# Performance work log

Measured on AMD Instinct MI355X. Metric: run time of the kernel, lower is better.

The kernel has to match this reference:

```python
import jax, jax.numpy as jnp
import numpy as np

T, LDIMS, HID, HID2 = 768, 256, 512, 512


def setup_inputs() -> dict:
    key = jax.random.key(0)
    ks = jax.random.split(key, 8)
    s = 0.05  # small init scale keeps tanh out of saturation
    return {
        "x": jax.random.normal(ks[0], (T, 2, LDIMS), dtype=jnp.float32),
        "hidLayerFOH": jax.random.normal(ks[1], (2 * LDIMS, HID), dtype=jnp.float32) * s,
        "hidLayerFOM": jax.random.normal(ks[2], (2 * LDIMS, HID), dtype=jnp.float32) * s,
        "catBias": jax.random.normal(ks[3], (2 * HID,), dtype=jnp.float32) * s,
        "hid2Layer": jax.random.normal(ks[4], (2 * HID, HID2), dtype=jnp.float32) * s,
        "hid2Bias": jax.random.normal(ks[5], (HID2,), dtype=jnp.float32) * s,
        "outLayer": jax.random.normal(ks[6], (HID2, 1), dtype=jnp.float32) * s,
        "outBias": jax.random.normal(ks[7], (1,), dtype=jnp.float32) * s,
    }


def reference(x, hidLayerFOH, hidLayerFOM, catBias, hid2Layer, hid2Bias, outLayer, outBias):
    # x: [T, 2, ldims] -> concat forward/backward LSTM states -> [T, 2*ldims]
    xc = x.reshape(x.shape[0], -1)
    Hf = xc @ hidLayerFOH  # [T, HID] headfov per token
    Mf = xc @ hidLayerFOM  # [T, HID] modfov per token
    # Original: tanh(concat([headfov_i, modfov_j]) + catBias) @ hid2Layer.
    # tanh is elementwise, so split the concat: act halves separately, then
    # split hid2Layer into top/bottom blocks — same math, no [T,T,2H] tensor.
    actH = jnp.tanh(Hf + catBias[:HID])   # [T, HID]
    actM = jnp.tanh(Mf + catBias[HID:])   # [T, HID]
    AH = actH @ hid2Layer[:HID]           # [T, HID2]
    AM = actM @ hid2Layer[HID:]           # [T, HID2]
    # Pairwise second layer: Z[i,j] = tanh(AH[i] + AM[j] + hid2Bias)
    Z = jnp.tanh(AH[:, None, :] + AM[None, :, :] + hid2Bias)  # [T, T, HID2]
    scores = jnp.einsum("ijh,h->ij", Z, outLayer[:, 0]) + outBias[0]  # [T, T]
    return scores
```

## Files before the change

### kernel.cpp

```cpp
#include <hip/hip_runtime.h>

#define TT 768
#define KD 512
#define NC 1024
#define RLN2_2 2.8853900817779268f

typedef short short8 __attribute__((ext_vector_type(8)));
typedef float f32x4  __attribute__((ext_vector_type(4)));
typedef float f32x2  __attribute__((ext_vector_type(2)));

__device__ __forceinline__ float fast_exp2(float x) {
#if __has_builtin(__builtin_amdgcn_exp2f)
    return __builtin_amdgcn_exp2f(x);
#else
    return exp2f(x);
#endif
}
__device__ __forceinline__ float fast_rcp(float x) {
#if __has_builtin(__builtin_amdgcn_rcpf)
    return __builtin_amdgcn_rcpf(x);
#else
    return 1.0f / x;
#endif
}
__device__ __forceinline__ float fast_tanh(float x) {
    float e = fast_exp2(x * RLN2_2);
    return fmaf(-2.0f, fast_rcp(e + 1.0f), 1.0f);
}
__device__ __forceinline__ ushort f2bf(float f) {
    uint u = __float_as_uint(f);
    u += 0x7fff + ((u >> 16) & 1);
    return (ushort)(u >> 16);
}

__global__ __launch_bounds__(64) void k_prep(
    const float* __restrict__ x, const float* __restrict__ foh,
    const float* __restrict__ fom, const float* __restrict__ hid2,
    ushort* __restrict__ xb, ushort* __restrict__ b1t, ushort* __restrict__ h2t)
{
    const int b = blockIdx.x, lane = threadIdx.x;
    if (b < 384) {
        int base = b * 1024 + lane * 16;
        #pragma unroll
        for (int q = 0; q < 4; ++q) {
            float4 v = *(const float4*)&x[base + q * 4];
            ushort4 o; o.x = f2bf(v.x); o.y = f2bf(v.y); o.z = f2bf(v.z); o.w = f2bf(v.w);
            *(ushort4*)&xb[base + q * 4] = o;
        }
        return;
    }
    __shared__ float tile[32][33];
    int bb = b - 384;
    const float* src; ushort* dst; int R, C;
    if (bb < 256)      { src = foh;  dst = b1t;             R = 512;  C = 512; }
    else if (bb < 512) { src = fom;  dst = b1t + 512 * 512; R = 512;  C = 512; bb -= 256; }
    else               { src = hid2; dst = h2t;             R = 1024; C = 512; bb -= 512; }
    const int r0 = (bb >> 4) * 32, c0 = (bb & 15) * 32;
    const int ty = lane >> 3, tx = lane & 7;
    #pragma unroll
    for (int q = 0; q < 4; ++q) {
        float4 v = *(const float4*)&src[(r0 + ty + q * 8) * C + c0 + tx * 4];
        tile[ty + q * 8][tx * 4 + 0] = v.x;
        tile[ty + q * 8][tx * 4 + 1] = v.y;
        tile[ty + q * 8][tx * 4 + 2] = v.z;
        tile[ty + q * 8][tx * 4 + 3] = v.w;
    }
    __syncthreads();
    #pragma unroll
    for (int q = 0; q < 4; ++q) {
        int cl = ty + q * 8;
        ushort4 o;
        o.x = f2bf(tile[tx * 4 + 0][cl]);
        o.y = f2bf(tile[tx * 4 + 1][cl]);
        o.z = f2bf(tile[tx * 4 + 2][cl]);
        o.w = f2bf(tile[tx * 4 + 3][cl]);
        *(ushort4*)&dst[(c0 + cl) * R + r0 + tx * 4] = o;
    }
}

__global__ __launch_bounds__(128) void k_gemm1(
    const ushort* __restrict__ xb, const ushort* __restrict__ b1t,
    const float* __restrict__ catBias, ushort* __restrict__ act)
{
    __shared__ float ps[64][20];
    const int t = threadIdx.x;
    const int kv = t >> 6, lane = t & 63;
    const int n0 = blockIdx.x * 32;
    const int m0 = blockIdx.y * 32;
    const int lrow = lane & 15, lk = (lane >> 4) * 8;
    const int kbase = kv * 256;

    const ushort* pa0 = &xb[(m0 + lrow) * KD + kbase + lk];
    const ushort* pa1 = pa0 + 16 * KD;
    const ushort* pb0 = &b1t[(n0 + lrow) * KD + kbase + lk];
    const ushort* pb1 = pb0 + 16 * KD;

    f32x4 acc[2][2] = {};
    #pragma unroll 4
    for (int k0 = 0; k0 < 256; k0 += 32) {
        short8 a0 = *(const short8*)(pa0 + k0);
        short8 a1 = *(const short8*)(pa1 + k0);
        short8 b0 = *(const short8*)(pb0 + k0);
        short8 b1 = *(const short8*)(pb1 + k0);
        acc[0][0] = __builtin_amdgcn_mfma_f32_16x16x32_bf16(a0, b0, acc[0][0], 0, 0, 0);
        acc[0][1] = __builtin_amdgcn_mfma_f32_16x16x32_bf16(a0, b1, acc[0][1], 0, 0, 0);
        acc[1][0] = __builtin_amdgcn_mfma_f32_16x16x32_bf16(a1, b0, acc[1][0], 0, 0, 0);
        acc[1][1] = __builtin_amdgcn_mfma_f32_16x16x32_bf16(a1, b1, acc[1][1], 0, 0, 0);
    }
    if (kv == 1) {
        *(f32x4*)&ps[lane][0]  = acc[0][0];
        *(f32x4*)&ps[lane][4]  = acc[0][1];
        *(f32x4*)&ps[lane][8]  = acc[1][0];
        *(f32x4*)&ps[lane][12] = acc[1][1];
    }
    __syncthreads();
    if (kv == 0) {
        acc[0][0] += *(const f32x4*)&ps[lane][0];
        acc[0][1] += *(const f32x4*)&ps[lane][4];
        acc[1][0] += *(const f32x4*)&ps[lane][8];
        acc[1][1] += *(const f32x4*)&ps[lane][12];
        const int crow = (lane >> 4) * 4, ccol = lane & 15;
        #pragma unroll
        for (int nf = 0; nf < 2; ++nf) {
            int col = n0 + nf * 16 + ccol;
            float cb = catBias[col];
            #pragma unroll
            for (int mf = 0; mf < 2; ++mf) {
                #pragma unroll
                for (int r = 0; r < 4; ++r) {
                    int row = m0 + mf * 16 + crow + r;
                    act[row * NC + col] = f2bf(fast_tanh(acc[mf][nf][r] + cb));
                }
            }
        }
    }
}

__global__ __launch_bounds__(128) void k_gemm2(
    const ushort* __restrict__ act, const ushort* __restrict__ h2t,
    const float* __restrict__ hid2Bias, float* __restrict__ pw)
{
    __shared__ float ps[64][20];
    const int t = threadIdx.x;
    const int kv = t >> 6, lane = t & 63;
    const int n0 = blockIdx.x * 32;
    const int m0 = blockIdx.y * 32;
    const bool top = (blockIdx.x < 16);
    const int koff = top ? 0 : 512;
    const int nc0  = top ? n0 : n0 - 512;
    const int lrow = lane & 15, lk = (lane >> 4) * 8;
    const int kbase = kv * 256;

    const ushort* pa0 = &act[(m0 + lrow) * NC + koff + kbase + lk];
    const ushort* pa1 = pa0 + 16 * NC;
    const ushort* pb0 = &h2t[(nc0 + lrow) * NC + koff + kbase + lk];
    const ushort* pb1 = pb0 + 16 * NC;

    f32x4 acc[2][2] = {};
    #pragma unroll 4
    for (int k0 = 0; k0 < 256; k0 += 32) {
        short8 a0 = *(const short8*)(pa0 + k0);
        short8 a1 = *(const short8*)(pa1 + k0);
        short8 b0 = *(const short8*)(pb0 + k0);
        short8 b1 = *(const short8*)(pb1 + k0);
        acc[0][0] = __builtin_amdgcn_mfma_f32_16x16x32_bf16(a0, b0, acc[0][0], 0, 0, 0);
        acc[0][1] = __builtin_amdgcn_mfma_f32_16x16x32_bf16(a0, b1, acc[0][1], 0, 0, 0);
        acc[1][0] = __builtin_amdgcn_mfma_f32_16x16x32_bf16(a1, b0, acc[1][0], 0, 0, 0);
        acc[1][1] = __builtin_amdgcn_mfma_f32_16x16x32_bf16(a1, b1, acc[1][1], 0, 0, 0);
    }
    if (kv == 1) {
        *(f32x4*)&ps[lane][0]  = acc[0][0];
        *(f32x4*)&ps[lane][4]  = acc[0][1];
        *(f32x4*)&ps[lane][8]  = acc[1][0];
        *(f32x4*)&ps[lane][12] = acc[1][1];
    }
    __syncthreads();
    if (kv == 0) {
        acc[0][0] += *(const f32x4*)&ps[lane][0];
        acc[0][1] += *(const f32x4*)&ps[lane][4];
        acc[1][0] += *(const f32x4*)&ps[lane][8];
        acc[1][1] += *(const f32x4*)&ps[lane][12];
        const int crow = (lane >> 4) * 4, ccol = lane & 15;
        #pragma unroll
        for (int nf = 0; nf < 2; ++nf) {
            int col = n0 + nf * 16 + ccol;
            float hb = top ? hid2Bias[col] : 0.0f;
            #pragma unroll
            for (int mf = 0; mf < 2; ++mf) {
                #pragma unroll
                for (int r = 0; r < 4; ++r) {
                    int row = m0 + mf * 16 + crow + r;
                    pw[row * NC + col] = fast_exp2(RLN2_2 * (acc[mf][nf][r] + hb));
                }
            }
        }
    }
}

__global__ __launch_bounds__(256) void k_pair(
    const float* __restrict__ pw, const float* __restrict__ w,
    const float* __restrict__ outBias, float* __restrict__ out)
{
    __shared__ float Ea[4][16][18];
    __shared__ float Em[4][16][18];
    __shared__ float wl[512];

    const int t    = threadIdx.x;
    const int wv   = t >> 6, lane = t & 63;
    const int bid  = blockIdx.x;
    const int sw   = (bid & 7) * 288 + (bid >> 3);
    const int it = sw / 48, jt = sw % 48;
    const int i0 = it * 16, j0 = jt * 16;
    const int hb0 = wv * 128;

    *(float2*)&wl[hb0 + lane * 2] = *(const float2*)&w[hb0 + lane * 2];
    float4 wa = *(const float4*)&w[lane * 8];
    float4 wb = *(const float4*)&w[lane * 8 + 4];
    float lsum = (wa.x + wa.y) + (wa.z + wa.w) + (wb.x + wb.y) + (wb.z + wb.w);
    #pragma unroll
    for (int d = 1; d < 64; d <<= 1) lsum += __shfl_xor(lsum, d, 64);

    const int sr = lane >> 2;
    const int sc = (lane & 3) * 4;
    const float* srcA = &pw[(i0 + sr) * NC + hb0 + sc];
    const float* srcM = &pw[(j0 + sr) * NC + 512 + hb0 + sc];

    const int li = lane >> 3, lj = lane & 7;

    float4 fa = *(const float4*)(srcA);
    float4 fm = *(const float4*)(srcM);

    const f32x2 one2 = {1.0f, 1.0f};
    f32x2 accA[2] = {}, accB[2] = {};

    #pragma unroll 1
    for (int c = 0; c < 8; ++c) {
        const int hh = c * 16;
        *(float4*)&Ea[wv][sr][sc] = fa;
        *(float4*)&Em[wv][sr][sc] = fm;
        if (c < 7) {
            fa = *(const float4*)(srcA + hh + 16);
            fm = *(const float4*)(srcM + hh + 16);
        }
        #pragma unroll
        for (int hq = 0; hq < 4; ++hq) {
            float4 e0 = *(const float4*)&Ea[wv][2 * li    ][hq * 4];
            float4 e1 = *(const float4*)&Ea[wv][2 * li + 1][hq * 4];
            float4 f0 = *(const float4*)&Em[wv][2 * lj    ][hq * 4];
            float4 f1 = *(const float4*)&Em[wv][2 * lj + 1][hq * 4];
            float4 w4 = *(const float4*)&wl[hb0 + hh + hq * 4];
            #define PKQUAD(DA, DB, WH, ACCA, ACCB)                   \
            {                                                        \
                f32x2 Q  = DA * DB;                                  \
                float pr = Q.x * Q.y;                                \
                float R  = fast_rcp(pr);                             \
                float RW = R * (WH);                                 \
                f32x2 T  = (f32x2){Q.y, Q.x} * RW;                   \
                ACCA = __builtin_elementwise_fma(T, DB, ACCA);       \
                ACCB = __builtin_elementwise_fma(T, DA, ACCB);       \
            }
            #define HSTEP(H, S)                                                     \
            {                                                                       \
                f32x2 F  = {f0.H, f1.H};                                            \
                f32x2 D0 = __builtin_elementwise_fma((f32x2){e0.H, e0.H}, F, one2); \
                f32x2 D1 = __builtin_elementwise_fma((f32x2){e1.H, e1.H}, F, one2); \
                PKQUAD(D0, D1, w4.H, accA[S], accB[S])                              \
            }
            HSTEP(x, 0) HSTEP(y, 1) HSTEP(z, 0) HSTEP(w, 1)
            #undef HSTEP
            #undef PKQUAD
        }
    }

    f32x2 s0 = accA[0] + accA[1];
    f32x2 s1 = accB[0] + accB[1];

    float* partial = (float*)Ea;
    __syncthreads();
    if (wv >= 1) {
        float* p = partial + (wv - 1) * 256 + lane * 4;
        p[0] = s0.x; p[1] = s0.y; p[2] = s1.x; p[3] = s1.y;
    }
    __syncthreads();
    if (wv == 0) {
        const float base = lsum + outBias[0];
        float t00 = s0.x, t01 = s0.y, t10 = s1.x, t11 = s1.y;
        #pragma unroll
        for (int q = 0; q < 3; ++q) {
            const float* p = partial + q * 256 + lane * 4;
            t00 += p[0]; t01 += p[1]; t10 += p[2]; t11 += p[3];
        }
        const int gi = i0 + 2 * li, gj = j0 + 2 * lj;
        float2 o0, o1;
        o0.x = fmaf(-2.f, t00, base);
        o0.y = fmaf(-2.f, t01, base);
        o1.x = fmaf(-2.f, t10, base);
        o1.y = fmaf(-2.f, t11, base);
        *(float2*)&out[gi * TT + gj]       = o0;
        *(float2*)&out[(gi + 1) * TT + gj] = o1;
    }
}

extern "C" void kernel_launch(void* const* d_in, const int* in_sizes, int n_in,
                              void* d_out, int out_size, void* d_ws, size_t ws_size,
                              hipStream_t stream) {
    const float* x        = (const float*)d_in[0];
    const float* foh      = (const float*)d_in[1];
    const float* fom      = (const float*)d_in[2];
    const float* catBias  = (const float*)d_in[3];
    const float* hid2     = (const float*)d_in[4];
    const float* hid2Bias = (const float*)d_in[5];
    const float* outLayer = (const float*)d_in[6];
    const float* outBias  = (const float*)d_in[7];
    float* out = (float*)d_out;

    char* wsb = (char*)d_ws;
    float*  pw  = (float*)(wsb);
    ushort* act = (ushort*)(wsb + 3145728);
    ushort* xb  = (ushort*)(wsb + 4718592);
    ushort* b1t = (ushort*)(wsb + 5505024);
    ushort* h2t = (ushort*)(wsb + 6553600);

    k_prep <<<dim3(1408),    64, 0, stream>>>(x, foh, fom, hid2, xb, b1t, h2t);
    k_gemm1<<<dim3(32, 24), 128, 0, stream>>>(xb, b1t, catBias, act);
    k_gemm2<<<dim3(32, 24), 128, 0, stream>>>(act, h2t, hid2Bias, pw);
    k_pair <<<dim3(2304),   256, 0, stream>>>(pw, outLayer, outBias, out);
}
```

Measured before the change: 58.84 us.

## Fuse bf16 conversion and weight transpose into GEMM loads, drop prep kernel

Removes the separate prep kernel that converted x and the weight matrices to bf16 and transposed them. Each GEMM now reads the fp32 weights directly, stages a 32x32 tile per wave in shared memory, and converts to bf16 while gathering the transposed MFMA operands; gemm1 also converts x on the fly. This cuts one kernel launch and the round trip of the converted copies through global memory. In exchange, the conversion and transpose are repeated in every row-block, and the k-loop is no longer unrolled, so load latency is less hidden.

```diff
diff --git a/kernel.cpp b/kernel.cpp
--- a/kernel.cpp
+++ b/kernel.cpp
@@ -33,79 +33,65 @@
     return (ushort)(u >> 16);
 }
 
-__global__ __launch_bounds__(64) void k_prep(
+__global__ __launch_bounds__(128) void k_gemm1(
     const float* __restrict__ x, const float* __restrict__ foh,
-    const float* __restrict__ fom, const float* __restrict__ hid2,
-    ushort* __restrict__ xb, ushort* __restrict__ b1t, ushort* __restrict__ h2t)
-{
-    const int b = blockIdx.x, lane = threadIdx.x;
-    if (b < 384) {
-        int base = b * 1024 + lane * 16;
-        #pragma unroll
-        for (int q = 0; q < 4; ++q) {
-            float4 v = *(const float4*)&x[base + q * 4];
-            ushort4 o; o.x = f2bf(v.x); o.y = f2bf(v.y); o.z = f2bf(v.z); o.w = f2bf(v.w);
-            *(ushort4*)&xb[base + q * 4] = o;
-        }
-        return;
-    }
-    __shared__ float tile[32][33];
-    int bb = b - 384;
-    const float* src; ushort* dst; int R, C;
-    if (bb < 256)      { src = foh;  dst = b1t;             R = 512;  C = 512; }
-    else if (bb < 512) { src = fom;  dst = b1t + 512 * 512; R = 512;  C = 512; bb -= 256; }
-    else               { src = hid2; dst = h2t;             R = 1024; C = 512; bb -= 512; }
-    const int r0 = (bb >> 4) * 32, c0 = (bb & 15) * 32;
-    const int ty = lane >> 3, tx = lane & 7;
-    #pragma unroll
-    for (int q = 0; q < 4; ++q) {
-        float4 v = *(const float4*)&src[(r0 + ty + q * 8) * C + c0 + tx * 4];
-        tile[ty + q * 8][tx * 4 + 0] = v.x;
-        tile[ty + q * 8][tx * 4 + 1] = v.y;
-        tile[ty + q * 8][tx * 4 + 2] = v.z;
-        tile[ty + q * 8][tx * 4 + 3] = v.w;
-    }
-    __syncthreads();
-    #pragma unroll
-    for (int q = 0; q < 4; ++q) {
-        int cl = ty + q * 8;
-        ushort4 o;
-        o.x = f2bf(tile[tx * 4 + 0][cl]);
-        o.y = f2bf(tile[tx * 4 + 1][cl]);
-        o.z = f2bf(tile[tx * 4 + 2][cl]);
-        o.w = f2bf(tile[tx * 4 + 3][cl]);
-        *(ushort4*)&dst[(c0 + cl) * R + r0 + tx * 4] = o;
-    }
-}
-
-__global__ __launch_bounds__(128) void k_gemm1(
-    const ushort* __restrict__ xb, const ushort* __restrict__ b1t,
-    const float* __restrict__ catBias, ushort* __restrict__ act)
+    const float* __restrict__ fom, const float* __restrict__ catBias,
+    ushort* __restrict__ act)
 {
     __shared__ float ps[64][20];
+    __shared__ float bt[2][32][33];
+
     const int t = threadIdx.x;
     const int kv = t >> 6, lane = t & 63;
     const int n0 = blockIdx.x * 32;
     const int m0 = blockIdx.y * 32;
+    const float* B = (n0 < 512) ? foh : fom;
+    const int nc0  = (n0 < 512) ? n0 : n0 - 512;
     const int lrow = lane & 15, lk = (lane >> 4) * 8;
     const int kbase = kv * 256;
 
-    const ushort* pa0 = &xb[(m0 + lrow) * KD + kbase + lk];
-    const ushort* pa1 = pa0 + 16 * KD;
-    const ushort* pb0 = &b1t[(n0 + lrow) * KD + kbase + lk];
-    const ushort* pb1 = pb0 + 16 * KD;
+    const int skr = lane >> 1;
+    const int snc = (lane & 1) * 16;
+
+    const float* px0 = &x[(m0 + lrow) * KD + kbase + lk];
+    const float* px1 = px0 + 16 * KD;
 
     f32x4 acc[2][2] = {};
-    #pragma unroll 4
-    for (int k0 = 0; k0 < 256; k0 += 32) {
-        short8 a0 = *(const short8*)(pa0 + k0);
-        short8 a1 = *(const short8*)(pa1 + k0);
-        short8 b0 = *(const short8*)(pb0 + k0);
-        short8 b1 = *(const short8*)(pb1 + k0);
-        acc[0][0] = __builtin_amdgcn_mfma_f32_16x16x32_bf16(a0, b0, acc[0][0], 0, 0, 0);
-        acc[0][1] = __builtin_amdgcn_mfma_f32_16x16x32_bf16(a0, b1, acc[0][1], 0, 0, 0);
-        acc[1][0] = __builtin_amdgcn_mfma_f32_16x16x32_bf16(a1, b0, acc[1][0], 0, 0, 0);
-        acc[1][1] = __builtin_amdgcn_mfma_f32_16x16x32_bf16(a1, b1, acc[1][1], 0, 0, 0);
+    #pragma unroll 1
+    for (int c = 0; c < 8; ++c) {
+        const int k0 = kbase + c * 32;
+        const float* bsrc = &B[(k0 + skr) * 512 + nc0 + snc];
+        float4 s0 = *(const float4*)(bsrc);
+        float4 s1 = *(const float4*)(bsrc + 4);
+        float4 s2 = *(const float4*)(bsrc + 8);
+        float4 s3 = *(const float4*)(bsrc + 12);
+        *(float4*)&bt[kv][skr][snc]      = s0;
+        *(float4*)&bt[kv][skr][snc + 4]  = s1;
+        *(float4*)&bt[kv][skr][snc + 8]  = s2;
+        *(float4*)&bt[kv][skr][snc + 12] = s3;
+        float4 a00 = *(const float4*)(px0 + c * 32);
+        float4 a01 = *(const float4*)(px0 + c * 32 + 4);
+        float4 a10 = *(const float4*)(px1 + c * 32);
+        float4 a11 = *(const float4*)(px1 + c * 32 + 4);
+        short8 af0, af1;
+        af0[0] = (short)f2bf(a00.x); af0[1] = (short)f2bf(a00.y);
+        af0[2] = (short)f2bf(a00.z); af0[3] = (short)f2bf(a00.w);
+        af0[4] = (short)f2bf(a01.x); af0[5] = (short)f2bf(a01.y);
+        af0[6] = (short)f2bf(a01.z); af0[7] = (short)f2bf(a01.w);
+        af1[0] = (short)f2bf(a10.x); af1[1] = (short)f2bf(a10.y);
+        af1[2] = (short)f2bf(a10.z); af1[3] = (short)f2bf(a10.w);
+        af1[4] = (short)f2bf(a11.x); af1[5] = (short)f2bf(a11.y);
+        af1[6] = (short)f2bf(a11.z); af1[7] = (short)f2bf(a11.w);
+        short8 bf0, bf1;
+        #pragma unroll
+        for (int q = 0; q < 8; ++q) {
+            bf0[q] = (short)f2bf(bt[kv][lk + q][lrow]);
+            bf1[q] = (short)f2bf(bt[kv][lk + q][lrow + 16]);
+        }
+        acc[0][0] = __builtin_amdgcn_mfma_f32_16x16x32_bf16(af0, bf0, acc[0][0], 0, 0, 0);
+        acc[0][1] = __builtin_amdgcn_mfma_f32_16x16x32_bf16(af0, bf1, acc[0][1], 0, 0, 0);
+        acc[1][0] = __builtin_amdgcn_mfma_f32_16x16x32_bf16(af1, bf0, acc[1][0], 0, 0, 0);
+        acc[1][1] = __builtin_amdgcn_mfma_f32_16x16x32_bf16(af1, bf1, acc[1][1], 0, 0, 0);
     }
     if (kv == 1) {
         *(f32x4*)&ps[lane][0]  = acc[0][0];
@@ -137,10 +123,12 @@
 }
 
 __global__ __launch_bounds__(128) void k_gemm2(
-    const ushort* __restrict__ act, const ushort* __restrict__ h2t,
+    const ushort* __restrict__ act, const float* __restrict__ hid2,
     const float* __restrict__ hid2Bias, float* __restrict__ pw)
 {
     __shared__ float ps[64][20];
+    __shared__ float bt[2][32][33];
+
     const int t = threadIdx.x;
     const int kv = t >> 6, lane = t & 63;
     const int n0 = blockIdx.x * 32;
@@ -151,22 +139,37 @@
     const int lrow = lane & 15, lk = (lane >> 4) * 8;
     const int kbase = kv * 256;
 
+    const int skr = lane >> 1;
+    const int snc = (lane & 1) * 16;
+
     const ushort* pa0 = &act[(m0 + lrow) * NC + koff + kbase + lk];
     const ushort* pa1 = pa0 + 16 * NC;
-    const ushort* pb0 = &h2t[(nc0 + lrow) * NC + koff + kbase + lk];
-    const ushort* pb1 = pb0 + 16 * NC;
 
     f32x4 acc[2][2] = {};
-    #pragma unroll 4
-    for (int k0 = 0; k0 < 256; k0 += 32) {
-        short8 a0 = *(const short8*)(pa0 + k0);
-        short8 a1 = *(const short8*)(pa1 + k0);
-        short8 b0 = *(const short8*)(pb0 + k0);
-        short8 b1 = *(const short8*)(pb1 + k0);
-        acc[0][0] = __builtin_amdgcn_mfma_f32_16x16x32_bf16(a0, b0, acc[0][0], 0, 0, 0);
-        acc[0][1] = __builtin_amdgcn_mfma_f32_16x16x32_bf16(a0, b1, acc[0][1], 0, 0, 0);
-        acc[1][0] = __builtin_amdgcn_mfma_f32_16x16x32_bf16(a1, b0, acc[1][0], 0, 0, 0);
-        acc[1][1] = __builtin_amdgcn_mfma_f32_16x16x32_bf16(a1, b1, acc[1][1], 0, 0, 0);
+    #pragma unroll 1
+    for (int c = 0; c < 8; ++c) {
+        const int k0 = kbase + c * 32;
+        const float* bsrc = &hid2[(koff + k0 + skr) * 512 + nc0 + snc];
+        float4 s0 = *(const float4*)(bsrc);
+        float4 s1 = *(const float4*)(bsrc + 4);
+        float4 s2 = *(const float4*)(bsrc + 8);
+        float4 s3 = *(const float4*)(bsrc + 12);
+        *(float4*)&bt[kv][skr][snc]      = s0;
+        *(float4*)&bt[kv][skr][snc + 4]  = s1;
+        *(float4*)&bt[kv][skr][snc + 8]  = s2;
+        *(float4*)&bt[kv][skr][snc + 12] = s3;
+        short8 af0 = *(const short8*)(pa0 + c * 32);
+        short8 af1 = *(const short8*)(pa1 + c * 32);
+        short8 bf0, bf1;
+        #pragma unroll
+        for (int q = 0; q < 8; ++q) {
+            bf0[q] = (short)f2bf(bt[kv][lk + q][lrow]);
+            bf1[q] = (short)f2bf(bt[kv][lk + q][lrow + 16]);
+        }
+        acc[0][0] = __builtin_amdgcn_mfma_f32_16x16x32_bf16(af0, bf0, acc[0][0], 0, 0, 0);
+        acc[0][1] = __builtin_amdgcn_mfma_f32_16x16x32_bf16(af0, bf1, acc[0][1], 0, 0, 0);
+        acc[1][0] = __builtin_amdgcn_mfma_f32_16x16x32_bf16(af1, bf0, acc[1][0], 0, 0, 0);
+        acc[1][1] = __builtin_amdgcn_mfma_f32_16x16x32_bf16(af1, bf1, acc[1][1], 0, 0, 0);
     }
     if (kv == 1) {
         *(f32x4*)&ps[lane][0]  = acc[0][0];
@@ -317,12 +320,8 @@
     char* wsb = (char*)d_ws;
     float*  pw  = (float*)(wsb);
     ushort* act = (ushort*)(wsb + 3145728);
-    ushort* xb  = (ushort*)(wsb + 4718592);
-    ushort* b1t = (ushort*)(wsb + 5505024);
-    ushort* h2t = (ushort*)(wsb + 6553600);
-
-    k_prep <<<dim3(1408),    64, 0, stream>>>(x, foh, fom, hid2, xb, b1t, h2t);
-    k_gemm1<<<dim3(32, 24), 128, 0, stream>>>(xb, b1t, catBias, act);
-    k_gemm2<<<dim3(32, 24), 128, 0, stream>>>(act, h2t, hid2Bias, pw);
+
+    k_gemm1<<<dim3(32, 24), 128, 0, stream>>>(x, foh, fom, catBias, act);
+    k_gemm2<<<dim3(32, 24), 128, 0, stream>>>(act, hid2, hid2Bias, pw);
     k_pair <<<dim3(2304),   256, 0, stream>>>(pw, outLayer, outBias, out);
 }
```

Result: faster. 55.37 us (median of 2 runs) (-5.9%).
